# Performance work log

Hardware: AMD Instinct MI355X
Metric: run time of the kernel (lower is better)

Reference implementation:

```python
import jax, jax.numpy as jnp
import numpy as np

EMBED = 1024
HEADS = 16
HEAD_DIM = EMBED // HEADS
MAX_SEQ = 5000
THETA = 10000.0
BATCH = 16
SEQ_K = 1024
SEQ_Q = 512


def _rope_tables():
    inv = 1.0 / (THETA ** (np.arange(0, EMBED, 2)[: EMBED // 2] / EMBED))
    ang = np.outer(np.arange(MAX_SEQ), inv)  # [MAX_SEQ, EMBED//2]
    return jnp.asarray(np.cos(ang), jnp.float32), jnp.asarray(np.sin(ang), jnp.float32)

COS_T, SIN_T = _rope_tables()


def _apply_rope(x, idx):
    # x: [B, S, E]; idx: [B, S]; pairs are (x[...,2i], x[...,2i+1]) across the FULL embed dim
    B, S, E = x.shape
    xp = x.reshape(B, S, E // 2, 2)
    xr, xi = xp[..., 0], xp[..., 1]
    c, s = COS_T[idx], SIN_T[idx]  # [B, S, E//2]
    return jnp.stack([xr * c - xi * s, xr * s + xi * c], axis=-1).reshape(B, S, E)


def _attn_mask(key_padding_mask):
    # (causal triu OR key padding) AND NOT eye  (eye keeps diagonal attendable), then cut query rows
    tri = jnp.triu(jnp.ones((SEQ_K, SEQ_K), bool), k=1)
    m = jnp.logical_or(tri[None], key_padding_mask[:, None, :])  # [B, K, K]
    m = jnp.logical_and(m, ~jnp.eye(SEQ_K, dtype=bool)[None])
    return m[:, -SEQ_Q:, :]  # [B, Q, K]


def setup_inputs() -> dict:
    key = jax.random.key(0)
    ks = jax.random.split(key, 16)
    def lin(i):
        W = jax.random.normal(ks[i], (EMBED, EMBED), jnp.float32) / np.sqrt(EMBED).astype(np.float32)
        b = jnp.zeros((EMBED,), jnp.float32)
        return W, b
    Wq, bq = lin(0); Wk, bk = lin(1); Wv, bv = lin(2); Wo, bo = lin(3)
    Wxr, bxr = lin(4); Wyr, byr = lin(5)
    Wxz, bxz = lin(6); Wyz, byz = lin(7)
    Wxg, bxg = lin(8); Wyg, byg = lin(9)
    key_in = jax.random.normal(ks[10], (BATCH, SEQ_K, EMBED), jnp.float32)
    key_index = jnp.sort(jax.random.randint(ks[11], (BATCH, SEQ_K), 0, MAX_SEQ), axis=-1)
    key_padding_mask = jax.random.randint(ks[12], (BATCH, SEQ_K), 0, 2).astype(bool)
    return dict(key_in=key_in, key_index=key_index, key_padding_mask=key_padding_mask,
                Wq=Wq, bq=bq, Wk=Wk, bk=bk, Wv=Wv, bv=bv, Wo=Wo, bo=bo,
                Wxr=Wxr, bxr=bxr, Wyr=Wyr, byr=byr, Wxz=Wxz, bxz=bxz,
                Wyz=Wyz, byz=byz, Wxg=Wxg, bxg=bxg, Wyg=Wyg, byg=byg)


def reference(key_in, key_index, key_padding_mask,
              Wq, bq, Wk, bk, Wv, bv, Wo, bo,
              Wxr, bxr, Wyr, byr, Wxz, bxz, Wyz, byz, Wxg, bxg, Wyg, byg):
    B = key_in.shape[0]
    # cut_query=True: query is the last SEQ_Q steps of key
    query = key_in[:, -SEQ_Q:]
    q_idx = key_index[:, -SEQ_Q:]
    q = query @ Wq + bq
    k = key_in @ Wk + bk
    v = key_in @ Wv + bv
    # RoPE applied on full embed dim BEFORE head split (as in source)
    q = _apply_rope(q, q_idx)
    k = _apply_rope(k, key_index)
    qh = q.reshape(B, SEQ_Q, HEADS, HEAD_DIM)
    kh = k.reshape(B, SEQ_K, HEADS, HEAD_DIM)
    vh = v.reshape(B, SEQ_K, HEADS, HEAD_DIM)
    mask = _attn_mask(key_padding_mask)  # [B, Q, K]
    bias = jnp.where(mask, -jnp.inf, 0.0).astype(key_in.dtype)[:, None]  # [B,1,Q,K]
    scores = jnp.einsum('bqhd,bkhd->bhqk', qh, kh) / np.float32(np.sqrt(HEAD_DIM)) + bias
    w = jax.nn.softmax(scores, axis=-1)  # [B,H,Q,K]
    o = jnp.einsum('bhqk,bkhd->bqhd', w, vh).reshape(B, SEQ_Q, EMBED)
    o = o @ Wo + bo
    # GRU-style gated residual combine (use_residual=True, use_gated=True)
    x = query
    r = jax.nn.sigmoid(x @ Wxr + bxr + o @ Wyr + byr)
    z = jax.nn.sigmoid(x @ Wxz + bxz + o @ Wyz + byz)
    h = jnp.tanh((r * x) @ Wxg + bxg + o @ Wyg + byg)
    out = (1.0 - z) * x + z * h
    attn_weights = w.mean(axis=1)  # averaged over heads, [B, Q, K]
    return out, attn_weights
```

## Files before the change

kernel.cpp:

```cpp
#include <hip/hip_runtime.h>
#include <hip/hip_bf16.h>


typedef __attribute__((ext_vector_type(8))) short bf16x8;
typedef __attribute__((ext_vector_type(4))) float f32x4;

__device__ __forceinline__ short f2bs(float f) {
  union { __hip_bfloat16 h; short s; } u; u.h = __float2bfloat16(f); return u.s;
}

static constexpr size_t OFF_WT   = 0;
static constexpr size_t OFF_TAB  = 20971520;
static constexpr size_t OFF_XBF  = 41451520;
static constexpr size_t OFF_QH   = 75005952;
static constexpr size_t OFF_KH   = 91783168;
static constexpr size_t OFF_VT   = 125337600;
static constexpr size_t OFF_OAT  = 158892032;
static constexpr size_t OFF_O2   = 175669248;
static constexpr size_t OFF_INV  = OFF_OAT;
static constexpr size_t OFF_RBZB = 75005952;
static constexpr size_t OFF_RX   = 142114816;
static constexpr size_t OFF_HB   = OFF_XBF;

__device__ __forceinline__ int swz(int q) { return ((q & 3) << 3) ^ ((q & 12) << 2); }

__global__ __launch_bounds__(256) void k_cvtx(const float* __restrict__ x,
                                              short* __restrict__ xbf) {
  size_t i = ((size_t)blockIdx.x * 256 + threadIdx.x) * 8;
  f32x4 a = *(const f32x4*)(x + i);
  f32x4 b = *(const f32x4*)(x + i + 4);
  bf16x8 o;
  o[0] = f2bs(a[0]); o[1] = f2bs(a[1]); o[2] = f2bs(a[2]); o[3] = f2bs(a[3]);
  o[4] = f2bs(b[0]); o[5] = f2bs(b[1]); o[6] = f2bs(b[2]); o[7] = f2bs(b[3]);
  *(bf16x8*)(xbf + i) = o;
}

__global__ void k_tabinv(double* __restrict__ inv) {
  int i = threadIdx.x;
  inv[i] = pow(10000.0, -(double)i / 512.0);
}
__global__ __launch_bounds__(256) void k_table(float* __restrict__ tab,
                                               const double* __restrict__ inv) {
  int i = blockIdx.x * 256 + threadIdx.x;
  if (i >= 5000 * 512) return;
  int pos = i >> 9, fi = i & 511;
  double ds, dc;
  sincos((double)pos * inv[fi], &ds, &dc);
  tab[2 * i] = (float)dc;
  tab[2 * i + 1] = (float)ds;
}

struct W10 { const float* p[10]; };
__global__ __launch_bounds__(256) void k_wt(W10 wsrc, short* __restrict__ wt) {
  __shared__ short t[32][33];
  int kb = blockIdx.x * 32, nb = blockIdx.y * 32, wi = blockIdx.z;
  const float* src = wsrc.p[wi];
  int tid = threadIdx.x;
#pragma unroll
  for (int e = 0; e < 4; ++e) {
    int idx = e * 256 + tid;
    int kr = idx >> 5, nc = idx & 31;
    t[nc][kr] = f2bs(src[(size_t)(kb + kr) * 1024 + nb + nc]);
  }
  __syncthreads();
  short* dst = wt + (size_t)wi * 1024 * 1024;
#pragma unroll
  for (int e = 0; e < 4; ++e) {
    int idx = e * 256 + tid;
    int nr = idx >> 5, kc = idx & 31;
    dst[(size_t)(nb + nr) * 1024 + kb + kc] = t[nr][kc];
  }
}

enum { CM_BF16 = 0, CM_F32 = 2, CM_F32ACC = 3, CM_VT = 4, CM_ROPE = 5 };

template <int AMODE, int CMODE>
__global__ __launch_bounds__(256) void k_gemm(
    const short* __restrict__ A, const short* __restrict__ Bt,
    const float* __restrict__ bias, const float* __restrict__ bias2,
    void* __restrict__ Cout, int ldc,
    const float* __restrict__ tab, const int* __restrict__ kidx,
    int sshift, int qoff) {
  __shared__ __align__(16) short lA[128 * 32];
  __shared__ __align__(16) short lB[128 * 32];
  const int tid = threadIdx.x;
  const int lane = tid & 63;
  const int wv = tid >> 6;
  const int wm = wv >> 1, wn = wv & 1;
  const int lo = lane & 15, hi = lane >> 4;
  const int tm0 = blockIdx.x * 128;
  const int tn0 = blockIdx.y * 128;

  const f32x4 vz = {0.f, 0.f, 0.f, 0.f};
  f32x4 acc[4][4];
#pragma unroll
  for (int m = 0; m < 4; ++m)
#pragma unroll
    for (int n = 0; n < 4; ++n) acc[m][n] = vz;

  for (int kt = 0; kt < 32; ++kt) {
    const int k0 = kt * 32;
    __syncthreads();
#pragma unroll
    for (int i = 0; i < 2; ++i) {
      int f = i * 256 + tid;
      int r = f >> 2;
      int cb = (f & 3) * 16;
      int arow = tm0 + r;
      if (AMODE) arow = ((arow >> 9) << 10) + 512 + (arow & 511);
      const char* ga = (const char*)(A + (size_t)arow * 1024 + k0) + cb;
      __builtin_amdgcn_global_load_lds(
          (const __attribute__((address_space(1))) void*)ga,
          (__attribute__((address_space(3))) void*)((char*)lA + (size_t)(i * 256 + wv * 64) * 16),
          16, 0, 0);
      int brow = tn0 + r;
      const char* gb = (const char*)(Bt + (size_t)brow * 1024 + k0) + cb;
      __builtin_amdgcn_global_load_lds(
          (const __attribute__((address_space(1))) void*)gb,
          (__attribute__((address_space(3))) void*)((char*)lB + (size_t)(i * 256 + wv * 64) * 16),
          16, 0, 0);
    }
    __syncthreads();
    bf16x8 af[4], bfr[4];
#pragma unroll
    for (int m = 0; m < 4; ++m)
      af[m] = *(const bf16x8*)&lA[(wm * 64 + m * 16 + lo) * 32 + hi * 8];
#pragma unroll
    for (int n = 0; n < 4; ++n)
      bfr[n] = *(const bf16x8*)&lB[(wn * 64 + n * 16 + lo) * 32 + hi * 8];
#pragma unroll
    for (int m = 0; m < 4; ++m)
#pragma unroll
      for (int n = 0; n < 4; ++n)
        acc[m][n] = __builtin_amdgcn_mfma_f32_16x16x32_bf16(af[m], bfr[n], acc[m][n], 0, 0, 0);
  }

  if constexpr (CMODE == CM_ROPE) {
    __hip_bfloat16* out = (__hip_bfloat16*)Cout;
    const float2* t2 = (const float2*)tab;
    const int srows = 1 << sshift;
    const float sgn = (lane & 1) ? 1.f : -1.f;
#pragma unroll
    for (int m = 0; m < 4; ++m) {
      int row_base = tm0 + wm * 64 + m * 16 + hi * 4;
#pragma unroll
      for (int n = 0; n < 4; ++n) {
        int col = tn0 + wn * 64 + n * 16 + lo;
        float bsv = bias[col];
        int j = col >> 1, hh = col >> 6, dd = col & 63;
#pragma unroll
        for (int r = 0; r < 4; ++r) {
          int row = row_base + r;
          int bb = row >> sshift, ss = row & (srows - 1);
          int idx = kidx[bb * 1024 + qoff + ss];
          float2 cs = t2[(size_t)idx * 512 + j];
          float val = acc[m][n][r] + bsv;
          float part = __shfl_xor(val, 1);
          float rot = val * cs.x + sgn * part * cs.y;
          out[((size_t)(bb * 16 + hh) * srows + ss) * 64 + dd] = __float2bfloat16(rot);
        }
      }
    }
  } else if constexpr (CMODE == CM_VT) {
    __hip_bfloat16* out = (__hip_bfloat16*)Cout;
#pragma unroll
    for (int m = 0; m < 4; ++m) {
      int row_base = tm0 + wm * 64 + m * 16 + hi * 4;
#pragma unroll
      for (int n = 0; n < 4; ++n) {
        int col = tn0 + wn * 64 + n * 16 + lo;
        float bsv = bias[col];
        int hh = col >> 6, dd = col & 63;
#pragma unroll
        for (int r = 0; r < 4; ++r) {
          int row = row_base + r;
          int bb = row >> 10, ss = row & 1023;
          out[((size_t)(bb * 16 + hh) * 64 + dd) * 1024 + ss] =
              __float2bfloat16(acc[m][n][r] + bsv);
        }
      }
    }
  } else if constexpr (CMODE == CM_F32 || CMODE == CM_F32ACC) {
    float* out = (float*)Cout;
#pragma unroll
    for (int m = 0; m < 4; ++m) {
      int row_base = tm0 + wm * 64 + m * 16 + hi * 4;
#pragma unroll
      for (int n = 0; n < 4; ++n) {
        int col = tn0 + wn * 64 + n * 16 + lo;
        float bsv = (col < 1024 || !bias2) ? bias[col] : bias2[col - 1024];
#pragma unroll
        for (int r = 0; r < 4; ++r) {
          size_t off = (size_t)(row_base + r) * ldc + col;
          float val = acc[m][n][r] + bsv;
          if constexpr (CMODE == CM_F32ACC) val += out[off];
          out[off] = val;
        }
      }
    }
  } else {
    __hip_bfloat16* out = (__hip_bfloat16*)Cout;
#pragma unroll
    for (int m = 0; m < 4; ++m) {
      int row_base = tm0 + wm * 64 + m * 16 + hi * 4;
#pragma unroll
      for (int n = 0; n < 4; ++n) {
        int col = tn0 + wn * 64 + n * 16 + lo;
        float bsv = bias[col];
#pragma unroll
        for (int r = 0; r < 4; ++r) {
          size_t off = (size_t)(row_base + r) * ldc + col;
          out[off] = __float2bfloat16(acc[m][n][r] + bsv);
        }
      }
    }
  }
}

__global__ __launch_bounds__(512, 2) void k_attn(
    const __hip_bfloat16* __restrict__ qh,
    const __hip_bfloat16* __restrict__ kh,
    const __hip_bfloat16* __restrict__ vt,
    const unsigned char* __restrict__ padraw,
    float* __restrict__ mean_out,
    __hip_bfloat16* __restrict__ oat) {
  __shared__ float Sld[16 * 1024];
  short* Pld = (short*)Sld;
  const int wgid = blockIdx.x;
  const int b = wgid & 15, qt = wgid >> 4;
  const int tid = threadIdx.x, lane = tid & 63, wv = tid >> 6;
  const int lo = lane & 15, hi = lane >> 4;
  const int wg = wv & 3, half = wv >> 2;
  const f32x4 vz = {0.f, 0.f, 0.f, 0.f};

  auto oscw = [&](int idx) -> float& { return Sld[(idx >> 9) * 1024 + (idx & 511)]; };

  bool is_byte = false;
#pragma unroll
  for (int j = 1; j < 256; ++j)
    if ((j & 3) && padraw[j] == 1) is_byte = true;
  const int* ipad = (const int*)padraw;

  unsigned pmask = 0;
#pragma unroll
  for (int nt = 0; nt < 8; ++nt) {
    int kpos = wv * 128 + nt * 16 + lo;
    int pk = is_byte ? (int)padraw[b * 1024 + kpos]
                     : (ipad[b * 1024 + kpos] != 0 ? 1 : 0);
    pmask |= (unsigned)(pk != 0) << nt;
  }

  float macc[2][16];
#pragma unroll
  for (int rr = 0; rr < 2; ++rr)
#pragma unroll
    for (int i = 0; i < 16; ++i) macc[rr][i] = 0.f;

  const __hip_bfloat16* qbase =
      qh + ((size_t)(b * 16) * 512 + (size_t)qt * 16) * 64;
  bf16x8 qf0 = *(const bf16x8*)(qbase + (size_t)lo * 64 + hi * 8);
  bf16x8 qf1 = *(const bf16x8*)(qbase + (size_t)lo * 64 + 32 + hi * 8);

  bf16x8 kb0[8], kb1[8];
  {
    const __hip_bfloat16* kbh0 = kh + (size_t)(b * 16) * 1024 * 64;
#pragma unroll
    for (int p = 0; p < 8; ++p) {
      int kr = wv * 128 + p * 16 + lo;
      kb0[p] = *(const bf16x8*)(kbh0 + (size_t)kr * 64 + hi * 8);
      kb1[p] = *(const bf16x8*)(kbh0 + (size_t)kr * 64 + 32 + hi * 8);
    }
  }

  for (int h = 0; h < 16; ++h) {
    const __hip_bfloat16* vrow =
        vt + ((size_t)(b * 16 + h) * 64 + wg * 16 + lo) * 1024;
    const int kcg = half * 16;

    bf16x8 vbuf[16];
#pragma unroll
    for (int nt = 0; nt < 8; ++nt) {
      vbuf[2 * nt]     = *(const bf16x8*)(vrow + (kcg + 2 * nt) * 32 + hi * 8);
      vbuf[2 * nt + 1] = *(const bf16x8*)(vrow + (kcg + 2 * nt + 1) * 32 + hi * 8);
      f32x4 sa = vz;
      sa = __builtin_amdgcn_mfma_f32_16x16x32_bf16(qf0, kb0[nt], sa, 0, 0, 0);
      sa = __builtin_amdgcn_mfma_f32_16x16x32_bf16(qf1, kb1[nt], sa, 0, 0, 0);
      int kpos = wv * 128 + nt * 16 + lo;
      int pk = (pmask >> nt) & 1;
#pragma unroll
      for (int r = 0; r < 4; ++r) {
        int q = hi * 4 + r;
        int qg = 512 + qt * 16 + q;
        float sv = sa[r] * 0.125f;
        bool msk = (kpos > qg) || (kpos < qg && pk != 0);
        Sld[q * 1024 + (kpos ^ swz(q))] = msk ? -1e30f : sv;
      }
    }
    __syncthreads();

#pragma unroll
    for (int rr = 0; rr < 2; ++rr) {
      int q = wv * 2 + rr;
      const int c = swz(q);
      float* row = Sld + q * 1024;
      float v[16], mx = -1e30f;
#pragma unroll
      for (int i = 0; i < 16; ++i) {
        v[i] = row[(lane + i * 64) ^ c];
        mx = fmaxf(mx, v[i]);
      }
#pragma unroll
      for (int off = 32; off > 0; off >>= 1) mx = fmaxf(mx, __shfl_xor(mx, off));
      float sum = 0.f;
#pragma unroll
      for (int i = 0; i < 16; ++i) { v[i] = __expf(v[i] - mx); sum += v[i]; }
#pragma unroll
      for (int off = 32; off > 0; off >>= 1) sum += __shfl_xor(sum, off);
      float invs = 1.0f / sum;
      short* prow = Pld + q * 2048 + 1024;
#pragma unroll
      for (int i = 0; i < 16; ++i) {
        float p = v[i] * invs;
        prow[(lane + i * 64) ^ c] = f2bs(p);
        macc[rr][i] += p;
      }
    }
    __syncthreads();

    f32x4 oacc = vz;
    {
      const short* prow = Pld + lo * 2048 + 1024;
      const int cl = swz(lo);
      const __hip_bfloat16* kbn =
          kh + (size_t)(b * 16 + (h < 15 ? h + 1 : h)) * 1024 * 64;
#pragma unroll
      for (int kc = 0; kc < 16; ++kc) {
        if (kc < 8 && h < 15) {
          int kr = wv * 128 + kc * 16 + lo;
          kb0[kc] = *(const bf16x8*)(kbn + (size_t)kr * 64 + hi * 8);
          kb1[kc] = *(const bf16x8*)(kbn + (size_t)kr * 64 + 32 + hi * 8);
        }
        bf16x8 pa = *(const bf16x8*)&prow[((kcg + kc) * 32 + hi * 8) ^ cl];
        oacc = __builtin_amdgcn_mfma_f32_16x16x32_bf16(pa, vbuf[kc], oacc, 0, 0, 0);
      }
    }

    if (h < 15) {
      const __hip_bfloat16* qn = qbase + (size_t)(h + 1) * 512 * 64;
      qf0 = *(const bf16x8*)(qn + (size_t)lo * 64 + hi * 8);
      qf1 = *(const bf16x8*)(qn + (size_t)lo * 64 + 32 + hi * 8);
    }

    if (half == 1) {
#pragma unroll
      for (int r = 0; r < 4; ++r) oscw((wg * 64 + lane) * 4 + r) = oacc[r];
    }
    __syncthreads();
    if (half == 0) {
#pragma unroll
      for (int r = 0; r < 4; ++r) {
        float o = oacc[r] + oscw((wg * 64 + lane) * 4 + r);
        int q = qt * 16 + hi * 4 + r;
        oat[((size_t)b * 512 + q) * 1024 + h * 64 + wg * 16 + lo] =
            __float2bfloat16(o);
      }
    }
    __syncthreads();
  }

#pragma unroll
  for (int rr = 0; rr < 2; ++rr) {
    size_t mrow = ((size_t)b * 512 + (size_t)qt * 16 + wv * 2 + rr) * 1024;
#pragma unroll
    for (int i = 0; i < 16; ++i)
      mean_out[mrow + lane + i * 64] = macc[rr][i] * 0.0625f;
  }
}

__global__ __launch_bounds__(256) void k_rx(const float* __restrict__ RbZb,
                                            const float* __restrict__ x,
                                            short* __restrict__ rx) {
  size_t base = ((size_t)blockIdx.x * 256 + threadIdx.x) * 4;
  int row = (int)(base >> 10), col = (int)(base & 1023);
  int b = row >> 9, s = row & 511;
  const float* xp = x + ((size_t)(b * 1024 + 512 + s) << 10) + col;
  f32x4 rv = *(const f32x4*)(RbZb + (size_t)row * 2048 + col);
  f32x4 xv = *(const f32x4*)xp;
  typedef __attribute__((ext_vector_type(4))) short s16x4;
  s16x4 o;
#pragma unroll
  for (int j = 0; j < 4; ++j) {
    float r = 1.f / (1.f + __expf(-rv[j]));
    o[j] = f2bs(r * xv[j]);
  }
  *(s16x4*)(rx + base) = o;
}

__global__ __launch_bounds__(256) void k_final(const float* __restrict__ RbZb,
                                               const float* __restrict__ Hb,
                                               const float* __restrict__ x,
                                               float* __restrict__ out0) {
  size_t base = ((size_t)blockIdx.x * 256 + threadIdx.x) * 4;
  int row = (int)(base >> 10), col = (int)(base & 1023);
  int b = row >> 9, s = row & 511;
  const float* xp = x + ((size_t)(b * 1024 + 512 + s) << 10) + col;
  f32x4 zv = *(const f32x4*)(RbZb + (size_t)row * 2048 + 1024 + col);
  f32x4 hv = *(const f32x4*)(Hb + base);
  f32x4 xv = *(const f32x4*)xp;
  f32x4 o;
#pragma unroll
  for (int j = 0; j < 4; ++j) {
    float z = 1.f / (1.f + __expf(-zv[j]));
    float hh = tanhf(hv[j]);
    o[j] = (1.f - z) * xv[j] + z * hh;
  }
  *(f32x4*)(out0 + base) = o;
}

extern "C" void kernel_launch(void* const* d_in, const int* in_sizes, int n_in,
                              void* d_out, int out_size, void* d_ws, size_t ws_size,
                              hipStream_t stream) {
  const float* key_in = (const float*)d_in[0];
  const int* key_index = (const int*)d_in[1];
  const unsigned char* pad = (const unsigned char*)d_in[2];
  const float* bq  = (const float*)d_in[4];
  const float* bk  = (const float*)d_in[6];
  const float* bv  = (const float*)d_in[8];
  const float* bo  = (const float*)d_in[10];
  const float* bxr = (const float*)d_in[12];
  const float* byr = (const float*)d_in[14];
  const float* bxz = (const float*)d_in[16];
  const float* byz = (const float*)d_in[18];
  const float* bxg = (const float*)d_in[20];
  const float* byg = (const float*)d_in[22];

  char* ws = (char*)d_ws;
  short* wt = (short*)(ws + OFF_WT);
  float* tab = (float*)(ws + OFF_TAB);
  short* xbf = (short*)(ws + OFF_XBF);
  __hip_bfloat16* qh = (__hip_bfloat16*)(ws + OFF_QH);
  __hip_bfloat16* kh = (__hip_bfloat16*)(ws + OFF_KH);
  __hip_bfloat16* vt = (__hip_bfloat16*)(ws + OFF_VT);
  double* inv = (double*)(ws + OFF_INV);
  float* RbZb = (float*)(ws + OFF_RBZB);
  __hip_bfloat16* oat = (__hip_bfloat16*)(ws + OFF_OAT);
  short* o2 = (short*)(ws + OFF_O2);
  short* rx = (short*)(ws + OFF_RX);
  float* Hb = (float*)(ws + OFF_HB);

  float* out0 = (float*)d_out;
  float* out1 = out0 + (size_t)8388608;

  W10 wargs;
  wargs.p[0] = (const float*)d_in[3];
  wargs.p[1] = (const float*)d_in[5];
  wargs.p[2] = (const float*)d_in[7];
  wargs.p[3] = (const float*)d_in[9];
  wargs.p[4] = (const float*)d_in[11];
  wargs.p[5] = (const float*)d_in[15];
  wargs.p[6] = (const float*)d_in[13];
  wargs.p[7] = (const float*)d_in[17];
  wargs.p[8] = (const float*)d_in[19];
  wargs.p[9] = (const float*)d_in[21];

  k_cvtx<<<8192, 256, 0, stream>>>(key_in, xbf);
  k_wt<<<dim3(32, 32, 10), 256, 0, stream>>>(wargs, wt);
  k_tabinv<<<1, 512, 0, stream>>>(inv);
  k_table<<<10000, 256, 0, stream>>>(tab, inv);

  k_gemm<1, CM_ROPE><<<dim3(64, 8), 256, 0, stream>>>(
      xbf, wt + (size_t)0 * 1048576, bq, nullptr, (void*)qh, 0, tab, key_index, 9, 512);
  k_gemm<0, CM_ROPE><<<dim3(128, 8), 256, 0, stream>>>(
      xbf, wt + (size_t)1 * 1048576, bk, nullptr, (void*)kh, 0, tab, key_index, 10, 0);
  k_gemm<0, CM_VT><<<dim3(128, 8), 256, 0, stream>>>(
      xbf, wt + (size_t)2 * 1048576, bv, nullptr, (void*)vt, 0, nullptr, nullptr, 0, 0);

  k_attn<<<dim3(512), 512, 0, stream>>>(qh, kh, vt, pad, out1, oat);

  k_gemm<0, CM_BF16><<<dim3(64, 8), 256, 0, stream>>>(
      (const short*)oat, wt + (size_t)3 * 1048576, bo, nullptr, (void*)o2, 1024,
      nullptr, nullptr, 0, 0);
  k_gemm<1, CM_F32><<<dim3(64, 16), 256, 0, stream>>>(
      xbf, wt + (size_t)4 * 1048576, bxr, bxz, (void*)RbZb, 2048,
      nullptr, nullptr, 0, 0);
  k_gemm<0, CM_F32ACC><<<dim3(64, 16), 256, 0, stream>>>(
      o2, wt + (size_t)6 * 1048576, byr, byz, (void*)RbZb, 2048,
      nullptr, nullptr, 0, 0);
  k_rx<<<8192, 256, 0, stream>>>(RbZb, key_in, rx);
  k_gemm<0, CM_F32><<<dim3(64, 8), 256, 0, stream>>>(
      rx, wt + (size_t)8 * 1048576, bxg, nullptr, (void*)Hb, 1024,
      nullptr, nullptr, 0, 0);
  k_gemm<0, CM_F32ACC><<<dim3(64, 8), 256, 0, stream>>>(
      o2, wt + (size_t)9 * 1048576, byg, nullptr, (void*)Hb, 1024,
      nullptr, nullptr, 0, 0);
  k_final<<<8192, 256, 0, stream>>>(RbZb, Hb, key_in, out0);
}
```

Measured before the change: 799.1 us.

## Shrink K/V register prefetch buffers and drop trailing barrier in attention loop

Replaces the whole-head register preload of K (16 vectors) and V (16 vectors), including the cross-head K prefetch, with 2-deep rolling double buffers loaded just ahead of each MFMA. This cuts register pressure, which may help sustain the 2-waves-per-SIMD launch bound. The partial-output exchange moves from the reused score buffer to a small dedicated shared array, which allows removing the final __syncthreads per head. In exchange, less load latency is hidden because V loads now come after softmax and K for the next head is no longer overlapped with the PV stage.

```diff
diff --git a/kernel.cpp b/kernel.cpp
--- a/kernel.cpp
+++ b/kernel.cpp
@@ -225,6 +225,7 @@
     float* __restrict__ mean_out,
     __hip_bfloat16* __restrict__ oat) {
   __shared__ float Sld[16 * 1024];
+  __shared__ float osc[4 * 64 * 4];
   short* Pld = (short*)Sld;
   const int wgid = blockIdx.x;
   const int b = wgid & 15, qt = wgid >> 4;
@@ -233,8 +234,6 @@
   const int wg = wv & 3, half = wv >> 2;
   const f32x4 vz = {0.f, 0.f, 0.f, 0.f};
 
-  auto oscw = [&](int idx) -> float& { return Sld[(idx >> 9) * 1024 + (idx & 511)]; };
-
   bool is_byte = false;
 #pragma unroll
   for (int j = 1; j < 256; ++j)
@@ -261,30 +260,28 @@
   bf16x8 qf0 = *(const bf16x8*)(qbase + (size_t)lo * 64 + hi * 8);
   bf16x8 qf1 = *(const bf16x8*)(qbase + (size_t)lo * 64 + 32 + hi * 8);
 
-  bf16x8 kb0[8], kb1[8];
-  {
-    const __hip_bfloat16* kbh0 = kh + (size_t)(b * 16) * 1024 * 64;
-#pragma unroll
-    for (int p = 0; p < 8; ++p) {
+  for (int h = 0; h < 16; ++h) {
+    const __hip_bfloat16* kbh = kh + (size_t)(b * 16 + h) * 1024 * 64;
+    const __hip_bfloat16* vbh = vt + (size_t)(b * 16 + h) * 64 * 1024;
+
+    bf16x8 kbuf[2][2];
+#pragma unroll
+    for (int p = 0; p < 2; ++p) {
       int kr = wv * 128 + p * 16 + lo;
-      kb0[p] = *(const bf16x8*)(kbh0 + (size_t)kr * 64 + hi * 8);
-      kb1[p] = *(const bf16x8*)(kbh0 + (size_t)kr * 64 + 32 + hi * 8);
-    }
-  }
-
-  for (int h = 0; h < 16; ++h) {
-    const __hip_bfloat16* vrow =
-        vt + ((size_t)(b * 16 + h) * 64 + wg * 16 + lo) * 1024;
-    const int kcg = half * 16;
-
-    bf16x8 vbuf[16];
+      kbuf[p][0] = *(const bf16x8*)(kbh + (size_t)kr * 64 + hi * 8);
+      kbuf[p][1] = *(const bf16x8*)(kbh + (size_t)kr * 64 + 32 + hi * 8);
+    }
 #pragma unroll
     for (int nt = 0; nt < 8; ++nt) {
-      vbuf[2 * nt]     = *(const bf16x8*)(vrow + (kcg + 2 * nt) * 32 + hi * 8);
-      vbuf[2 * nt + 1] = *(const bf16x8*)(vrow + (kcg + 2 * nt + 1) * 32 + hi * 8);
+      bf16x8 ck0 = kbuf[nt & 1][0], ck1 = kbuf[nt & 1][1];
+      if (nt < 6) {
+        int kr = wv * 128 + (nt + 2) * 16 + lo;
+        kbuf[nt & 1][0] = *(const bf16x8*)(kbh + (size_t)kr * 64 + hi * 8);
+        kbuf[nt & 1][1] = *(const bf16x8*)(kbh + (size_t)kr * 64 + 32 + hi * 8);
+      }
       f32x4 sa = vz;
-      sa = __builtin_amdgcn_mfma_f32_16x16x32_bf16(qf0, kb0[nt], sa, 0, 0, 0);
-      sa = __builtin_amdgcn_mfma_f32_16x16x32_bf16(qf1, kb1[nt], sa, 0, 0, 0);
+      sa = __builtin_amdgcn_mfma_f32_16x16x32_bf16(qf0, ck0, sa, 0, 0, 0);
+      sa = __builtin_amdgcn_mfma_f32_16x16x32_bf16(qf1, ck1, sa, 0, 0, 0);
       int kpos = wv * 128 + nt * 16 + lo;
       int pk = (pmask >> nt) & 1;
 #pragma unroll
@@ -331,17 +328,19 @@
     {
       const short* prow = Pld + lo * 2048 + 1024;
       const int cl = swz(lo);
-      const __hip_bfloat16* kbn =
-          kh + (size_t)(b * 16 + (h < 15 ? h + 1 : h)) * 1024 * 64;
+      const int kcg = half * 16;
+      const __hip_bfloat16* vrow = vbh + (size_t)(wg * 16 + lo) * 1024;
+      bf16x8 vbuf[2];
+#pragma unroll
+      for (int p = 0; p < 2; ++p)
+        vbuf[p] = *(const bf16x8*)(vrow + (kcg + p) * 32 + hi * 8);
 #pragma unroll
       for (int kc = 0; kc < 16; ++kc) {
-        if (kc < 8 && h < 15) {
-          int kr = wv * 128 + kc * 16 + lo;
-          kb0[kc] = *(const bf16x8*)(kbn + (size_t)kr * 64 + hi * 8);
-          kb1[kc] = *(const bf16x8*)(kbn + (size_t)kr * 64 + 32 + hi * 8);
-        }
+        bf16x8 cv = vbuf[kc & 1];
+        if (kc < 14)
+          vbuf[kc & 1] = *(const bf16x8*)(vrow + (kcg + kc + 2) * 32 + hi * 8);
         bf16x8 pa = *(const bf16x8*)&prow[((kcg + kc) * 32 + hi * 8) ^ cl];
-        oacc = __builtin_amdgcn_mfma_f32_16x16x32_bf16(pa, vbuf[kc], oacc, 0, 0, 0);
+        oacc = __builtin_amdgcn_mfma_f32_16x16x32_bf16(pa, cv, oacc, 0, 0, 0);
       }
     }
 
@@ -353,19 +352,18 @@
 
     if (half == 1) {
 #pragma unroll
-      for (int r = 0; r < 4; ++r) oscw((wg * 64 + lane) * 4 + r) = oacc[r];
+      for (int r = 0; r < 4; ++r) osc[(wg * 64 + lane) * 4 + r] = oacc[r];
     }
     __syncthreads();
     if (half == 0) {
 #pragma unroll
       for (int r = 0; r < 4; ++r) {
-        float o = oacc[r] + oscw((wg * 64 + lane) * 4 + r);
+        float o = oacc[r] + osc[(wg * 64 + lane) * 4 + r];
         int q = qt * 16 + hi * 4 + r;
         oat[((size_t)b * 512 + q) * 1024 + h * 64 + wg * 16 + lo] =
             __float2bfloat16(o);
       }
     }
-    __syncthreads();
   }
 
 #pragma unroll
```

Result: faster. 768.4 us (median of 3 runs) (-3.8%).
